# Kernel optimization log

Measured on AMD Instinct MI355X. Metric: run time of the kernel, lower is better.

The kernel has to match this reference:

```python
import jax, jax.numpy as jnp
import numpy as np

SCALE = 20.0
THRESHOLD = 0.9995


def setup_inputs() -> dict:
    key = jax.random.key(0)
    k1, k2, k3 = jax.random.split(key, 3)
    B, C, H, W, S = 4, 128, 96, 128, 1024
    # L2-normalize along channel so the dot product is a true cosine in [-1, 1]
    # (keeps exp(scale * (x - threshold)) numerically sane, as intended by the module).
    def unit(x):
        return x / (jnp.linalg.norm(x, axis=1, keepdims=True) + 1e-8)
    source_feature_map = unit(jax.random.normal(k1, (B, C, H, W), dtype=jnp.float32))
    target_feature_map = unit(jax.random.normal(k2, (B, C, H, W), dtype=jnp.float32))
    source_feature_1D_locations = jax.random.randint(k3, (B, S, 1), 0, H * W, dtype=jnp.int64)
    mask = jnp.ones((B, 1, H, W), dtype=jnp.float32)
    return {
        "source_feature_map": source_feature_map,
        "target_feature_map": target_feature_map,
        "source_feature_1D_locations": source_feature_1D_locations,
        "mask": mask,
    }


def reference(source_feature_map, target_feature_map, source_feature_1D_locations, mask):
    B, C, H, W = source_feature_map.shape
    loc = source_feature_1D_locations[..., 0]  # [B, S]
    src_flat = source_feature_map.reshape(B, C, H * W)  # [B, C, HW]
    # gather sampled query vectors: [B, C, S]
    sampled = jnp.take_along_axis(src_flat, loc[:, None, :], axis=2)
    # per-batch 1x1 conv == batched matmul: [B, S, H, W]
    corr = jnp.einsum('bchw,bcs->bshw', target_feature_map, sampled)
    resp = jnp.exp(SCALE * (0.5 * corr + 0.5 - THRESHOLD)) * mask  # mask broadcasts [B,1,H,W]
    resp = resp / jnp.sum(resp, axis=(2, 3), keepdims=True)
    return resp
```

## Files before the change

kernel.cpp:

```cpp
#include <hip/hip_runtime.h>

typedef unsigned int u32;
typedef unsigned short u16;
typedef short s8v __attribute__((ext_vector_type(8)));
typedef float f16v __attribute__((ext_vector_type(16)));

#define NB 4
#define NC 128
#define HW 12288
#define NS 1024

#define EXP_A 10.0f
#define EXP_B (-9.99f)

__device__ inline u16 f2bf(float f) {
    u32 u = __float_as_uint(f);
    u32 r = u + 0x7fffu + ((u >> 16) & 1u);
    return (u16)(r >> 16);
}
__device__ inline float bf2f(u16 h) { return __uint_as_float(((u32)h) << 16); }

__global__ __launch_bounds__(256) void prep_samp(
    const float* __restrict__ src, const int* __restrict__ loc,
    u16* __restrict__ shi, u16* __restrict__ slo, float* __restrict__ sums)
{
    int t = threadIdx.x;
    int gid = blockIdx.x * 256 + t;
    if (gid < NB * NS) sums[gid] = 0.0f;
    int bs = blockIdx.x * 2 + (t >> 7);
    int c  = t & 127;
    int b  = bs >> 10;
    int l  = loc[bs];
    float v = src[((size_t)(b * NC + c)) * HW + l];
    u16 h  = f2bf(v);
    u16 lo = f2bf(v - bf2f(h));
    shi[bs * NC + c] = h;
    slo[bs * NC + c] = lo;
}

__global__ __launch_bounds__(256) void prep_tgt(
    const float* __restrict__ tgt, u16* __restrict__ bhi, u16* __restrict__ blo)
{
    __shared__ float tile[NC][65];
    int b = blockIdx.y, pt = blockIdx.x, t = threadIdx.x;
    const float* src = tgt + ((size_t)b * NC) * HW + pt * 64;
#pragma unroll
    for (int it = 0; it < 32; ++it) {
        int idx = it * 256 + t;
        int c = idx >> 6, px = idx & 63;
        tile[c][px] = src[(size_t)c * HW + px];
    }
    __syncthreads();
    int px = t >> 2, cq = (t & 3) * 32;
    u32 hw_[16], lw_[16];
#pragma unroll
    for (int k = 0; k < 16; ++k) {
        float v0 = tile[cq + 2 * k][px], v1 = tile[cq + 2 * k + 1][px];
        u16 h0 = f2bf(v0), h1 = f2bf(v1);
        u16 l0 = f2bf(v0 - bf2f(h0)), l1 = f2bf(v1 - bf2f(h1));
        hw_[k] = (u32)h0 | ((u32)h1 << 16);
        lw_[k] = (u32)l0 | ((u32)l1 << 16);
    }
    size_t rowbase = ((size_t)b * HW + pt * 64 + px) * NC + cq;
    uint4* ph = (uint4*)(bhi + rowbase);
    uint4* pl = (uint4*)(blo + rowbase);
#pragma unroll
    for (int q = 0; q < 4; ++q) {
        ph[q] = make_uint4(hw_[4*q], hw_[4*q+1], hw_[4*q+2], hw_[4*q+3]);
        pl[q] = make_uint4(lw_[4*q], lw_[4*q+1], lw_[4*q+2], lw_[4*q+3]);
    }
}

template <int DO_STORE>
__global__ __launch_bounds__(256) void corr_mfma(
    const u16* __restrict__ bhi, const u16* __restrict__ blo,
    const u16* __restrict__ shi, const u16* __restrict__ slo,
    const float* __restrict__ mask, float* __restrict__ sums,
    float* __restrict__ out)
{
    __shared__ char smem[33792];
    __shared__ float inv[256];
    u16*   Bt = (u16*)smem;
    float* rs = (float*)smem;

    const int b = blockIdx.z, st = blockIdx.y, pt = blockIdx.x;
    const int t = threadIdx.x, w = t >> 6, l = t & 63;
    const int h = l >> 5, ln = l & 31;

    {
        const u16* g0 = bhi + ((size_t)b * HW + pt * 64) * NC;
        const u16* g1 = blo + ((size_t)b * HW + pt * 64) * NC;
#pragma unroll
        for (int p = 0; p < 2; ++p) {
            const u16* gs = p ? g1 : g0;
#pragma unroll
            for (int it = 0; it < 4; ++it) {
                int g = it * 256 + t;
                int px = g >> 4, kg = g & 15;
                uint4 v = *(const uint4*)(gs + g * 8);
                int swz = (kg & 8) | ((kg ^ px) & 7);
                *(uint4*)&Bt[p * 64 * NC + px * NC + swz * 8] = v;
            }
        }
    }
    if (DO_STORE) {
        inv[t] = 1.0f / sums[b * NS + st * 256 + t];
    }
    __syncthreads();

    f16v acc[2][2];
#pragma unroll
    for (int i = 0; i < 2; ++i)
#pragma unroll
        for (int j = 0; j < 2; ++j)
#pragma unroll
            for (int r = 0; r < 16; ++r) acc[i][j][r] = 0.0f;

    const int srow0 = st * 256 + w * 64 + ln;
    const u16* ah = shi + ((size_t)(b * NS) + srow0) * NC + h * 8;
    const u16* al = slo + ((size_t)(b * NS) + srow0) * NC + h * 8;

#pragma unroll
    for (int kk = 0; kk < 8; ++kk) {
        s8v a_hi[2], a_lo[2], b_hi[2], b_lo[2];
#pragma unroll
        for (int i = 0; i < 2; ++i) {
            a_hi[i] = *(const s8v*)(ah + i * 32 * NC + kk * 16);
            a_lo[i] = *(const s8v*)(al + i * 32 * NC + kk * 16);
        }
        int kg = kk * 2 + h;
#pragma unroll
        for (int j = 0; j < 2; ++j) {
            int px = j * 32 + ln;
            int swz = (kg & 8) | ((kg ^ px) & 7);
            b_hi[j] = *(const s8v*)&Bt[0 * 64 * NC + px * NC + swz * 8];
            b_lo[j] = *(const s8v*)&Bt[1 * 64 * NC + px * NC + swz * 8];
        }
#pragma unroll
        for (int i = 0; i < 2; ++i)
#pragma unroll
            for (int j = 0; j < 2; ++j) {
                acc[i][j] = __builtin_amdgcn_mfma_f32_32x32x16_bf16(a_hi[i], b_hi[j], acc[i][j], 0, 0, 0);
                acc[i][j] = __builtin_amdgcn_mfma_f32_32x32x16_bf16(a_lo[i], b_hi[j], acc[i][j], 0, 0, 0);
                acc[i][j] = __builtin_amdgcn_mfma_f32_32x32x16_bf16(a_hi[i], b_lo[j], acc[i][j], 0, 0, 0);
            }
    }

    float mv[2];
#pragma unroll
    for (int j = 0; j < 2; ++j) mv[j] = mask[(size_t)b * HW + pt * 64 + j * 32 + ln];

    if (DO_STORE) {
#pragma unroll
        for (int i = 0; i < 2; ++i) {
            int rbase = w * 64 + i * 32 + 4 * h;
#pragma unroll
            for (int j = 0; j < 2; ++j) {
                float* obase = out + ((size_t)(b * NS) + st * 256) * HW + (size_t)pt * 64 + j * 32 + ln;
#pragma unroll
                for (int r = 0; r < 16; ++r) {
                    int row = rbase + (r & 3) + 8 * (r >> 2);
                    float e = __expf(fmaf(acc[i][j][r], EXP_A, EXP_B)) * mv[j];
                    obase[(size_t)row * HW] = e * inv[row];
                }
            }
        }
    } else {
        __syncthreads();
#pragma unroll
        for (int i = 0; i < 2; ++i) {
            int rbase = w * 64 + i * 32 + 4 * h;
#pragma unroll
            for (int r = 0; r < 16; ++r) {
                int row = rbase + (r & 3) + 8 * (r >> 2);
                float e0 = __expf(fmaf(acc[i][0][r], EXP_A, EXP_B)) * mv[0];
                float e1 = __expf(fmaf(acc[i][1][r], EXP_A, EXP_B)) * mv[1];
                rs[row * 33 + ln] = e0 + e1;
            }
        }
        __syncthreads();
        float tot = 0.0f;
#pragma unroll
        for (int c = 0; c < 32; ++c) tot += rs[t * 33 + c];
        atomicAdd(&sums[b * NS + st * 256 + t], tot);
    }
}

extern "C" void kernel_launch(void* const* d_in, const int* in_sizes, int n_in,
                              void* d_out, int out_size, void* d_ws, size_t ws_size,
                              hipStream_t stream) {
    const float* src  = (const float*)d_in[0];
    const float* tgt  = (const float*)d_in[1];
    const int*   loc  = (const int*)d_in[2];
    const float* mask = (const float*)d_in[3];
    float* out = (float*)d_out;

    char* ws = (char*)d_ws;
    const size_t PLANE = (size_t)NB * HW * NC * sizeof(u16);
    const size_t SPLANE = (size_t)NB * NS * NC * sizeof(u16);
    u16* bhi = (u16*)ws;
    u16* blo = (u16*)(ws + PLANE);
    u16* shi = (u16*)(ws + 2 * PLANE);
    u16* slo = (u16*)(ws + 2 * PLANE + SPLANE);
    float* sums = (float*)(ws + 2 * PLANE + 2 * SPLANE);

    prep_samp<<<dim3(NB * NS / 2), 256, 0, stream>>>(src, loc, shi, slo, sums);
    prep_tgt<<<dim3(HW / 64, NB), 256, 0, stream>>>(tgt, bhi, blo);

    dim3 g(HW / 64, NS / 256, NB);
    corr_mfma<0><<<g, 256, 0, stream>>>(bhi, blo, shi, slo, mask, sums, out);
    corr_mfma<1><<<g, 256, 0, stream>>>(bhi, blo, shi, slo, mask, sums, out);
}
```

Baseline: 360.0 us.

## Restructure correlation kernel into larger 256x256 tiles with direct-to-LDS K-chunked loads

Replaces the 256x64 tile GEMM with a 512-thread kernel that computes 256 samples by 256 pixels per block. A and B operands are reorganised into K-chunked, XOR-swizzled layouts and streamed into LDS with global_load_lds. The grid is flattened and remapped so that blocks sharing operand tiles land on the same XCD. prep_tgt drops its LDS transpose and writes the new layout directly. The larger tiles are meant to cut redundant operand loads, at the cost of more registers per thread and fewer blocks in flight.

```diff
diff --git a/kernel.cpp b/kernel.cpp
--- a/kernel.cpp
+++ b/kernel.cpp
@@ -13,176 +13,187 @@
 #define EXP_A 10.0f
 #define EXP_B (-9.99f)
 
+#define TS 256
+#define TP 256
+#define NPT (HW/TP)
+#define NST (NS/TS)
+
 __device__ inline u16 f2bf(float f) {
     u32 u = __float_as_uint(f);
-    u32 r = u + 0x7fffu + ((u >> 16) & 1u);
-    return (u16)(r >> 16);
+    return (u16)((u + 0x7fffu + ((u >> 16) & 1u)) >> 16);
 }
 __device__ inline float bf2f(u16 h) { return __uint_as_float(((u32)h) << 16); }
+
+__device__ inline void gload_lds16(const void* g, void* l) {
+    __builtin_amdgcn_global_load_lds(
+        (const __attribute__((address_space(1))) void*)g,
+        (__attribute__((address_space(3))) void*)l, 16, 0, 0);
+}
 
 __global__ __launch_bounds__(256) void prep_samp(
     const float* __restrict__ src, const int* __restrict__ loc,
-    u16* __restrict__ shi, u16* __restrict__ slo, float* __restrict__ sums)
+    u16* __restrict__ ahi, u16* __restrict__ alo, float* __restrict__ sums)
 {
     int t = threadIdx.x;
     int gid = blockIdx.x * 256 + t;
     if (gid < NB * NS) sums[gid] = 0.0f;
     int bs = blockIdx.x * 2 + (t >> 7);
     int c  = t & 127;
-    int b  = bs >> 10;
+    int b  = bs >> 10, s = bs & 1023;
     int l  = loc[bs];
     float v = src[((size_t)(b * NC + c)) * HW + l];
     u16 h  = f2bf(v);
     u16 lo = f2bf(v - bf2f(h));
-    shi[bs * NC + c] = h;
-    slo[bs * NC + c] = lo;
+    int kc = c >> 5, u = (c >> 3) & 3, e = c & 7;
+    int slot = u ^ ((s >> 1) & 3);
+    size_t off = ((size_t)((b * 4 + kc) * NS + s)) * 32 + slot * 8 + e;
+    ahi[off] = h;
+    alo[off] = lo;
 }
 
 __global__ __launch_bounds__(256) void prep_tgt(
     const float* __restrict__ tgt, u16* __restrict__ bhi, u16* __restrict__ blo)
 {
-    __shared__ float tile[NC][65];
     int b = blockIdx.y, pt = blockIdx.x, t = threadIdx.x;
-    const float* src = tgt + ((size_t)b * NC) * HW + pt * 64;
-#pragma unroll
-    for (int it = 0; it < 32; ++it) {
-        int idx = it * 256 + t;
-        int c = idx >> 6, px = idx & 63;
-        tile[c][px] = src[(size_t)c * HW + px];
-    }
-    __syncthreads();
-    int px = t >> 2, cq = (t & 3) * 32;
-    u32 hw_[16], lw_[16];
-#pragma unroll
-    for (int k = 0; k < 16; ++k) {
-        float v0 = tile[cq + 2 * k][px], v1 = tile[cq + 2 * k + 1][px];
-        u16 h0 = f2bf(v0), h1 = f2bf(v1);
-        u16 l0 = f2bf(v0 - bf2f(h0)), l1 = f2bf(v1 - bf2f(h1));
-        hw_[k] = (u32)h0 | ((u32)h1 << 16);
-        lw_[k] = (u32)l0 | ((u32)l1 << 16);
-    }
-    size_t rowbase = ((size_t)b * HW + pt * 64 + px) * NC + cq;
-    uint4* ph = (uint4*)(bhi + rowbase);
-    uint4* pl = (uint4*)(blo + rowbase);
-#pragma unroll
-    for (int q = 0; q < 4; ++q) {
-        ph[q] = make_uint4(hw_[4*q], hw_[4*q+1], hw_[4*q+2], hw_[4*q+3]);
-        pl[q] = make_uint4(lw_[4*q], lw_[4*q+1], lw_[4*q+2], lw_[4*q+3]);
+    int pxl = t & 63, u = t >> 6;
+    int px = pt * 64 + pxl;
+    int slot = u ^ ((px >> 1) & 3);
+#pragma unroll
+    for (int kc = 0; kc < 4; ++kc) {
+        int c0 = kc * 32 + u * 8;
+        u32 hq[4], lq[4];
+#pragma unroll
+        for (int k = 0; k < 4; ++k) {
+            float v0 = tgt[((size_t)(b * NC + c0 + 2 * k)) * HW + px];
+            float v1 = tgt[((size_t)(b * NC + c0 + 2 * k + 1)) * HW + px];
+            u16 h0 = f2bf(v0), h1 = f2bf(v1);
+            u16 l0 = f2bf(v0 - bf2f(h0)), l1 = f2bf(v1 - bf2f(h1));
+            hq[k] = (u32)h0 | ((u32)h1 << 16);
+            lq[k] = (u32)l0 | ((u32)l1 << 16);
+        }
+        size_t off = (((size_t)((b * 4 + kc) * HW + px)) * 4 + slot) * 8;
+        *(uint4*)(bhi + off) = make_uint4(hq[0], hq[1], hq[2], hq[3]);
+        *(uint4*)(blo + off) = make_uint4(lq[0], lq[1], lq[2], lq[3]);
     }
 }
 
 template <int DO_STORE>
-__global__ __launch_bounds__(256) void corr_mfma(
+__global__ __launch_bounds__(512) void corr2(
     const u16* __restrict__ bhi, const u16* __restrict__ blo,
-    const u16* __restrict__ shi, const u16* __restrict__ slo,
+    const u16* __restrict__ ahi, const u16* __restrict__ alo,
     const float* __restrict__ mask, float* __restrict__ sums,
     float* __restrict__ out)
 {
-    __shared__ char smem[33792];
-    __shared__ float inv[256];
-    u16*   Bt = (u16*)smem;
-    float* rs = (float*)smem;
-
-    const int b = blockIdx.z, st = blockIdx.y, pt = blockIdx.x;
-    const int t = threadIdx.x, w = t >> 6, l = t & 63;
-    const int h = l >> 5, ln = l & 31;
-
-    {
-        const u16* g0 = bhi + ((size_t)b * HW + pt * 64) * NC;
-        const u16* g1 = blo + ((size_t)b * HW + pt * 64) * NC;
-#pragma unroll
-        for (int p = 0; p < 2; ++p) {
-            const u16* gs = p ? g1 : g0;
-#pragma unroll
-            for (int it = 0; it < 4; ++it) {
-                int g = it * 256 + t;
-                int px = g >> 4, kg = g & 15;
-                uint4 v = *(const uint4*)(gs + g * 8);
-                int swz = (kg & 8) | ((kg ^ px) & 7);
-                *(uint4*)&Bt[p * 64 * NC + px * NC + swz * 8] = v;
-            }
-        }
-    }
+    __shared__ __align__(1024) char sm[65536];
+    __shared__ float inv[TS];
+
+    int f = blockIdx.x;
+    int xcd = f & 7, r0 = f >> 3;
+    int st = r0 & 3;
+    int p  = (r0 >> 2) * 8 + xcd;
+    int b  = p / 48, pt = p - b * 48;
+
+    int t = threadIdx.x, w = t >> 6, l = t & 63, ln = l & 31, h = l >> 5;
+    int ws = w >> 1, wp = w & 1;
+
     if (DO_STORE) {
-        inv[t] = 1.0f / sums[b * NS + st * 256 + t];
-    }
-    __syncthreads();
-
-    f16v acc[2][2];
+        if (t < TS) inv[t] = 1.0f / sums[b * NS + st * TS + t];
+    }
+
+    f16v acc[2][4];
 #pragma unroll
     for (int i = 0; i < 2; ++i)
 #pragma unroll
-        for (int j = 0; j < 2; ++j)
+        for (int j = 0; j < 4; ++j)
 #pragma unroll
             for (int r = 0; r < 16; ++r) acc[i][j][r] = 0.0f;
 
-    const int srow0 = st * 256 + w * 64 + ln;
-    const u16* ah = shi + ((size_t)(b * NS) + srow0) * NC + h * 8;
-    const u16* al = slo + ((size_t)(b * NS) + srow0) * NC + h * 8;
-
-#pragma unroll
-    for (int kk = 0; kk < 8; ++kk) {
-        s8v a_hi[2], a_lo[2], b_hi[2], b_lo[2];
+    for (int kc = 0; kc < 4; ++kc) {
+        const char* ga_h = (const char*)ahi + ((size_t)((b * 4 + kc) * NS + st * TS)) * 64;
+        const char* ga_l = (const char*)alo + ((size_t)((b * 4 + kc) * NS + st * TS)) * 64;
+        const char* gb_h = (const char*)bhi + ((size_t)((b * 4 + kc) * HW + pt * TP)) * 64;
+        const char* gb_l = (const char*)blo + ((size_t)((b * 4 + kc) * HW + pt * TP)) * 64;
+#pragma unroll
+        for (int it = 0; it < 8; ++it) {
+            int q = w * 8 + it;
+            int rg = q >> 4, inner = q & 15;
+            const char* gb = rg == 0 ? ga_h : rg == 1 ? ga_l : rg == 2 ? gb_h : gb_l;
+            gload_lds16(gb + inner * 1024 + l * 16, sm + q * 1024);
+        }
+        __syncthreads();
+
+#pragma unroll
+        for (int kk2 = 0; kk2 < 2; ++kk2) {
+            int u = kk2 * 2 + h;
+            s8v a_h[2], a_l[2], b_h[4], b_l[4];
+#pragma unroll
+            for (int i = 0; i < 2; ++i) {
+                int row = ws * 64 + i * 32 + ln;
+                int sl = u ^ ((row >> 1) & 3);
+                a_h[i] = *(const s8v*)(sm + 0 * 16384 + row * 64 + sl * 16);
+                a_l[i] = *(const s8v*)(sm + 1 * 16384 + row * 64 + sl * 16);
+            }
+#pragma unroll
+            for (int j = 0; j < 4; ++j) {
+                int px = wp * 128 + j * 32 + ln;
+                int sl = u ^ ((px >> 1) & 3);
+                b_h[j] = *(const s8v*)(sm + 2 * 16384 + px * 64 + sl * 16);
+                b_l[j] = *(const s8v*)(sm + 3 * 16384 + px * 64 + sl * 16);
+            }
+#pragma unroll
+            for (int i = 0; i < 2; ++i)
+#pragma unroll
+                for (int j = 0; j < 4; ++j) {
+                    acc[i][j] = __builtin_amdgcn_mfma_f32_32x32x16_bf16(a_h[i], b_h[j], acc[i][j], 0, 0, 0);
+                    acc[i][j] = __builtin_amdgcn_mfma_f32_32x32x16_bf16(a_l[i], b_h[j], acc[i][j], 0, 0, 0);
+                    acc[i][j] = __builtin_amdgcn_mfma_f32_32x32x16_bf16(a_h[i], b_l[j], acc[i][j], 0, 0, 0);
+                }
+        }
+        __syncthreads();
+    }
+
+    float mv[4];
+#pragma unroll
+    for (int j = 0; j < 4; ++j)
+        mv[j] = mask[(size_t)b * HW + pt * TP + wp * 128 + j * 32 + ln];
+
+    if (DO_STORE) {
+        float* ob0 = out + ((size_t)(b * NS + st * TS)) * HW + pt * TP + wp * 128 + ln;
 #pragma unroll
         for (int i = 0; i < 2; ++i) {
-            a_hi[i] = *(const s8v*)(ah + i * 32 * NC + kk * 16);
-            a_lo[i] = *(const s8v*)(al + i * 32 * NC + kk * 16);
-        }
-        int kg = kk * 2 + h;
-#pragma unroll
-        for (int j = 0; j < 2; ++j) {
-            int px = j * 32 + ln;
-            int swz = (kg & 8) | ((kg ^ px) & 7);
-            b_hi[j] = *(const s8v*)&Bt[0 * 64 * NC + px * NC + swz * 8];
-            b_lo[j] = *(const s8v*)&Bt[1 * 64 * NC + px * NC + swz * 8];
-        }
-#pragma unroll
-        for (int i = 0; i < 2; ++i)
-#pragma unroll
-            for (int j = 0; j < 2; ++j) {
-                acc[i][j] = __builtin_amdgcn_mfma_f32_32x32x16_bf16(a_hi[i], b_hi[j], acc[i][j], 0, 0, 0);
-                acc[i][j] = __builtin_amdgcn_mfma_f32_32x32x16_bf16(a_lo[i], b_hi[j], acc[i][j], 0, 0, 0);
-                acc[i][j] = __builtin_amdgcn_mfma_f32_32x32x16_bf16(a_hi[i], b_lo[j], acc[i][j], 0, 0, 0);
-            }
-    }
-
-    float mv[2];
-#pragma unroll
-    for (int j = 0; j < 2; ++j) mv[j] = mask[(size_t)b * HW + pt * 64 + j * 32 + ln];
-
-    if (DO_STORE) {
+            int rb = ws * 64 + i * 32 + 4 * h;
+#pragma unroll
+            for (int j = 0; j < 4; ++j) {
+#pragma unroll
+                for (int r = 0; r < 16; ++r) {
+                    int row = rb + (r & 3) + 8 * (r >> 2);
+                    float e = __expf(fmaf(acc[i][j][r], EXP_A, EXP_B)) * mv[j];
+                    ob0[(size_t)row * HW + j * 32] = e * inv[row];
+                }
+            }
+        }
+    } else {
+        float* rs = (float*)sm;
 #pragma unroll
         for (int i = 0; i < 2; ++i) {
-            int rbase = w * 64 + i * 32 + 4 * h;
-#pragma unroll
-            for (int j = 0; j < 2; ++j) {
-                float* obase = out + ((size_t)(b * NS) + st * 256) * HW + (size_t)pt * 64 + j * 32 + ln;
-#pragma unroll
-                for (int r = 0; r < 16; ++r) {
-                    int row = rbase + (r & 3) + 8 * (r >> 2);
-                    float e = __expf(fmaf(acc[i][j][r], EXP_A, EXP_B)) * mv[j];
-                    obase[(size_t)row * HW] = e * inv[row];
-                }
-            }
-        }
-    } else {
+            int rb = ws * 64 + i * 32 + 4 * h;
+#pragma unroll
+            for (int r = 0; r < 16; ++r) {
+                int row = rb + (r & 3) + 8 * (r >> 2);
+                float e = 0.0f;
+#pragma unroll
+                for (int j = 0; j < 4; ++j)
+                    e += __expf(fmaf(acc[i][j][r], EXP_A, EXP_B)) * mv[j];
+                rs[(wp * TS + row) * 32 + ln] = e;
+            }
+        }
         __syncthreads();
-#pragma unroll
-        for (int i = 0; i < 2; ++i) {
-            int rbase = w * 64 + i * 32 + 4 * h;
-#pragma unroll
-            for (int r = 0; r < 16; ++r) {
-                int row = rbase + (r & 3) + 8 * (r >> 2);
-                float e0 = __expf(fmaf(acc[i][0][r], EXP_A, EXP_B)) * mv[0];
-                float e1 = __expf(fmaf(acc[i][1][r], EXP_A, EXP_B)) * mv[1];
-                rs[row * 33 + ln] = e0 + e1;
-            }
-        }
-        __syncthreads();
+        int row = t & 255, half = t >> 8;
         float tot = 0.0f;
 #pragma unroll
-        for (int c = 0; c < 32; ++c) tot += rs[t * 33 + c];
-        atomicAdd(&sums[b * NS + st * 256 + t], tot);
+        for (int c = 0; c < 32; ++c)
+            tot += rs[(half * TS + row) * 32 + ((c + t) & 31)];
+        atomicAdd(&sums[b * NS + st * TS + row], tot);
     }
 }
 
@@ -196,18 +207,18 @@
     float* out = (float*)d_out;
 
     char* ws = (char*)d_ws;
-    const size_t PLANE = (size_t)NB * HW * NC * sizeof(u16);
-    const size_t SPLANE = (size_t)NB * NS * NC * sizeof(u16);
+    const size_t BPLANE = (size_t)NB * 4 * HW * 32 * sizeof(u16);
+    const size_t APLANE = (size_t)NB * 4 * NS * 32 * sizeof(u16);
     u16* bhi = (u16*)ws;
-    u16* blo = (u16*)(ws + PLANE);
-    u16* shi = (u16*)(ws + 2 * PLANE);
-    u16* slo = (u16*)(ws + 2 * PLANE + SPLANE);
-    float* sums = (float*)(ws + 2 * PLANE + 2 * SPLANE);
-
-    prep_samp<<<dim3(NB * NS / 2), 256, 0, stream>>>(src, loc, shi, slo, sums);
+    u16* blo = (u16*)(ws + BPLANE);
+    u16* ahi = (u16*)(ws + 2 * BPLANE);
+    u16* alo = (u16*)(ws + 2 * BPLANE + APLANE);
+    float* sums = (float*)(ws + 2 * BPLANE + 2 * APLANE);
+
+    prep_samp<<<dim3(NB * NS / 2), 256, 0, stream>>>(src, loc, ahi, alo, sums);
     prep_tgt<<<dim3(HW / 64, NB), 256, 0, stream>>>(tgt, bhi, blo);
 
-    dim3 g(HW / 64, NS / 256, NB);
-    corr_mfma<0><<<g, 256, 0, stream>>>(bhi, blo, shi, slo, mask, sums, out);
-    corr_mfma<1><<<g, 256, 0, stream>>>(bhi, blo, shi, slo, mask, sums, out);
-}
+    dim3 g(NPT * NST * NB);
+    corr2<0><<<g, 512, 0, stream>>>(bhi, blo, ahi, alo, mask, sums, out);
+    corr2<1><<<g, 512, 0, stream>>>(bhi, blo, ahi, alo, mask, sums, out);
+}
```

Result: faster. 323.5 us (-10.1%).
